# Kernel tuning notes

Measured on AMD Instinct MI355X. Metric: run time of the kernel, lower is better.

Reference implementation:

```python
import jax, jax.numpy as jnp
import numpy as np

B, S, H, A, E = 64, 1024, 1024, 512, 512


def setup_inputs() -> dict:
    key = jax.random.key(0)
    ks = jax.random.split(key, 13)
    sc = 0.02
    return {
        "inputs": jax.random.normal(ks[0], (B, E), jnp.float32),
        "states": jax.random.normal(ks[1], (B, H), jnp.float32),
        "encoded": jax.random.normal(ks[2], (B, S, H), jnp.float32),
        "W_enc": jax.random.normal(ks[3], (H, A), jnp.float32) * sc,
        "b_enc": jax.random.normal(ks[4], (A,), jnp.float32) * sc,
        "W_dec": jax.random.normal(ks[5], (H, A), jnp.float32) * sc,
        "b_dec": jax.random.normal(ks[6], (A,), jnp.float32) * sc,
        "w_out": jax.random.normal(ks[7], (A,), jnp.float32) * sc,
        "b_out": jax.random.normal(ks[8], (1,), jnp.float32) * sc,
        "W_ih": jax.random.normal(ks[9], (E + H, 3 * H), jnp.float32) * sc,
        "b_ih": jax.random.normal(ks[10], (3 * H,), jnp.float32) * sc,
        "W_hh": jax.random.normal(ks[11], (H, 3 * H), jnp.float32) * sc,
        "b_hh": jax.random.normal(ks[12], (3 * H,), jnp.float32) * sc,
    }


def reference(inputs, states, encoded, W_enc, b_enc, W_dec, b_dec, w_out, b_out,
              W_ih, b_ih, W_hh, b_hh):
    # setup_memory: project encoder states once  [B,S,H] @ [H,A] -> [B,S,A]
    enc_proj = jnp.einsum('bsh,ha->bsa', encoded, W_enc) + b_enc
    # Bahdanau additive attention
    dec_proj = states @ W_dec + b_dec                       # [B,A]
    scores = jnp.einsum('bsa,a->bs', jnp.tanh(enc_proj + dec_proj[:, None, :]), w_out) + b_out[0]
    weights = jax.nn.softmax(scores, axis=1)                # [B,S]
    attention = jnp.einsum('bs,bsh->bh', weights, encoded)  # [B,H]
    x = jnp.concatenate([inputs, attention], axis=-1)       # [B,E+H]
    # GRUCell (PyTorch gate order r, z, n)
    gi = x @ W_ih + b_ih                                    # [B,3H]
    gh = states @ W_hh + b_hh                               # [B,3H]
    i_r, i_z, i_n = jnp.split(gi, 3, axis=-1)
    h_r, h_z, h_n = jnp.split(gh, 3, axis=-1)
    r = jax.nn.sigmoid(i_r + h_r)
    z = jax.nn.sigmoid(i_z + h_z)
    n = jnp.tanh(i_n + r * h_n)
    h_new = (1.0 - z) * n + z * states
    return h_new
```

## Files before the change

kernel.cpp:

```cpp
#include <hip/hip_runtime.h>
#include <hip/hip_bf16.h>


typedef __attribute__((ext_vector_type(8))) __bf16 bf16x8;
typedef __attribute__((ext_vector_type(4))) __bf16 bf16x4;
typedef __attribute__((ext_vector_type(4))) float f32x4;

__device__ __forceinline__ float fast_tanh(float x) {
  float xa = fminf(fmaxf(x, -15.f), 15.f);
  float e = __expf(2.f * xa);
  return (e - 1.f) / (e + 1.f);
}

__global__ __launch_bounds__(256) void wenc_t_kernel(const float* __restrict__ W,
                                                     __bf16* __restrict__ Wt) {
  __shared__ float tile[32][33];
  int k0 = blockIdx.x * 32, a0 = blockIdx.y * 32;
  int tid = threadIdx.x;
  int r = tid >> 3, c4 = (tid & 7) * 4;
  f32x4 v = *(const f32x4*)(W + (long)(k0 + r) * 512 + a0 + c4);
  tile[r][c4 + 0] = v.x; tile[r][c4 + 1] = v.y;
  tile[r][c4 + 2] = v.z; tile[r][c4 + 3] = v.w;
  __syncthreads();
  int a = tid >> 3, k4 = (tid & 7) * 4;
  bf16x4 o = { (__bf16)tile[k4 + 0][a], (__bf16)tile[k4 + 1][a],
               (__bf16)tile[k4 + 2][a], (__bf16)tile[k4 + 3][a] };
  *(bf16x4*)(Wt + (long)(a0 + a) * 1024 + k0 + k4) = o;
}

__global__ __launch_bounds__(256) void dec_proj_kernel(
    const float* __restrict__ states, const float* __restrict__ W_dec,
    const float* __restrict__ b_enc, const float* __restrict__ b_dec,
    float* __restrict__ addv) {
  int b = blockIdx.x, tid = threadIdx.x;
  int a = blockIdx.y * 256 + tid;
  __shared__ float sl[1024];
  for (int i = tid; i < 1024; i += 256) sl[i] = states[b * 1024 + i];
  __syncthreads();
  float c0 = 0.f, c1 = 0.f, c2 = 0.f, c3 = 0.f;
#pragma unroll 4
  for (int i = 0; i < 256; ++i) {
    c0 += sl[i]         * W_dec[(i)        * 512 + a];
    c1 += sl[i + 256]   * W_dec[(i + 256)  * 512 + a];
    c2 += sl[i + 512]   * W_dec[(i + 512)  * 512 + a];
    c3 += sl[i + 768]   * W_dec[(i + 768)  * 512 + a];
  }
  addv[b * 512 + a] = c0 + c1 + c2 + c3 + b_enc[a] + b_dec[a];
}

struct Stage { f32x4 a[4]; bf16x8 b[2]; };

__global__ __launch_bounds__(512, 4) void enc_score_kernel(
    const float* __restrict__ encoded,
    const __bf16* __restrict__ Wt,
    const float* __restrict__ addv,
    const float* __restrict__ w_out,
    float* __restrict__ psc)
{
  __shared__ __attribute__((aligned(16))) char smem[65536];
  float* red = (float*)smem;

  const int d = blockIdx.x;
  const int xcd = d & 7;
  const int slot = d >> 3;
  const int bn = slot & 3;
  const int bm = ((slot >> 2) << 3) | xcd;

  const int tid = threadIdx.x;
  const int lane = tid & 63;
  const int wid = tid >> 6;
  const int wrow = wid >> 2;
  const int wcol = wid & 3;
  const int lr = lane & 15;
  const int lkb = lane >> 4;

  const long row0 = (long)bm * 128;
  const int col0 = bn * 128;

  const int arow = tid >> 2, akq = tid & 3;
  const int bcol = tid >> 2, bkq = tid & 3;
  const float* aBase = encoded + (row0 + arow) * 1024 + akq * 16;
  const __bf16* bBase = Wt + (long)(col0 + bcol) * 1024 + bkq * 16;
  const int asw = (arow & 7) << 4;
  const int aw0 = arow * 128 + ((akq * 32) ^ asw);
  const int aw1 = arow * 128 + ((akq * 32 + 16) ^ asw);
  const int bsw = (bcol & 7) << 4;
  const int bw0 = bcol * 128 + ((bkq * 32) ^ bsw);
  const int bw1 = bcol * 128 + ((bkq * 32 + 16) ^ bsw);

  const int rdSw = (lkb << 4) ^ ((lr & 7) << 4);
  const int aRow = (wrow * 64 + lr) * 128;
  const int bRow = (wcol * 32 + lr) * 128;

  f32x4 acc[4][2];
#pragma unroll
  for (int m = 0; m < 4; ++m)
#pragma unroll
    for (int n = 0; n < 2; ++n) acc[m][n] = (f32x4){0.f, 0.f, 0.f, 0.f};

  Stage X, Y;

#define ISSUE(S, KT) do { \
    _Pragma("unroll") for (int _j = 0; _j < 4; ++_j) \
      S.a[_j] = *(const f32x4*)(aBase + (KT) * 64 + _j * 4); \
    _Pragma("unroll") for (int _j = 0; _j < 2; ++_j) \
      S.b[_j] = *(const bf16x8*)(bBase + (KT) * 64 + _j * 8); \
    __builtin_amdgcn_sched_barrier(0); \
  } while (0)

#define STORE(S, ABUF) do { \
    bf16x8 _w0, _w1; \
    _Pragma("unroll") for (int _i = 0; _i < 4; ++_i) { \
      _w0[_i] = (__bf16)S.a[0][_i]; _w0[_i + 4] = (__bf16)S.a[1][_i]; \
      _w1[_i] = (__bf16)S.a[2][_i]; _w1[_i + 4] = (__bf16)S.a[3][_i]; } \
    *(bf16x8*)(smem + (ABUF) + aw0) = _w0; \
    *(bf16x8*)(smem + (ABUF) + aw1) = _w1; \
    *(bf16x8*)(smem + 32768 + (ABUF) + bw0) = S.b[0]; \
    *(bf16x8*)(smem + 32768 + (ABUF) + bw1) = S.b[1]; \
    __builtin_amdgcn_sched_barrier(0); \
  } while (0)

#define COMPUTE(ABUF) do { \
    _Pragma("unroll") for (int _ks = 0; _ks < 2; ++_ks) { \
      bf16x8 _af[4], _bf[2]; \
      _Pragma("unroll") for (int _m = 0; _m < 4; ++_m) \
        _af[_m] = *(const bf16x8*)(smem + (ABUF) + aRow + _m * 2048 + (rdSw ^ (_ks << 6))); \
      _Pragma("unroll") for (int _n = 0; _n < 2; ++_n) \
        _bf[_n] = *(const bf16x8*)(smem + 32768 + (ABUF) + bRow + _n * 2048 + (rdSw ^ (_ks << 6))); \
      asm volatile("s_waitcnt lgkmcnt(0)" ::: "memory"); \
      __builtin_amdgcn_sched_barrier(0); \
      __builtin_amdgcn_s_setprio(1); \
      _Pragma("unroll") for (int _m = 0; _m < 4; ++_m) \
        _Pragma("unroll") for (int _n = 0; _n < 2; ++_n) \
          acc[_m][_n] = __builtin_amdgcn_mfma_f32_16x16x32_bf16(_af[_m], _bf[_n], acc[_m][_n], 0, 0, 0); \
      __builtin_amdgcn_s_setprio(0); \
      __builtin_amdgcn_sched_barrier(0); \
    } \
  } while (0)

#define BAR() do { \
    asm volatile("s_waitcnt lgkmcnt(0)" ::: "memory"); \
    __builtin_amdgcn_sched_barrier(0); \
    __builtin_amdgcn_s_barrier(); \
    __builtin_amdgcn_sched_barrier(0); \
  } while (0)

  ISSUE(X, 0);
  ISSUE(Y, 1);
  STORE(X, 0);
  BAR();

  for (int t2 = 0; t2 < 7; ++t2) {
    ISSUE(X, 2 * t2 + 2);
    COMPUTE(0);
    STORE(Y, 16384);
    BAR();
    ISSUE(Y, 2 * t2 + 3);
    COMPUTE(16384);
    STORE(X, 0);
    BAR();
  }
  COMPUTE(0);
  STORE(Y, 16384);
  BAR();
  COMPUTE(16384);

#undef ISSUE
#undef STORE
#undef COMPUTE
#undef BAR

  const int b = bm >> 3;
  const float* addvb = addv + b * 512;
  float rowsum[4][4];
#pragma unroll
  for (int m = 0; m < 4; ++m)
#pragma unroll
    for (int reg = 0; reg < 4; ++reg) rowsum[m][reg] = 0.f;

#pragma unroll
  for (int m = 0; m < 4; ++m) {
#pragma unroll
    for (int n = 0; n < 2; ++n) {
      int col = col0 + wcol * 32 + n * 16 + lr;
      float av = addvb[col];
      float wo = w_out[col];
#pragma unroll
      for (int reg = 0; reg < 4; ++reg)
        rowsum[m][reg] += fast_tanh(acc[m][n][reg] + av) * wo;
    }
  }
#pragma unroll
  for (int m = 0; m < 4; ++m)
#pragma unroll
    for (int reg = 0; reg < 4; ++reg) {
      float v = rowsum[m][reg];
      v += __shfl_xor(v, 1, 64);
      v += __shfl_xor(v, 2, 64);
      v += __shfl_xor(v, 4, 64);
      v += __shfl_xor(v, 8, 64);
      rowsum[m][reg] = v;
    }
  if (lr == 0) {
#pragma unroll
    for (int m = 0; m < 4; ++m)
#pragma unroll
      for (int reg = 0; reg < 4; ++reg)
        red[(wrow * 64 + m * 16 + lkb * 4 + reg) * 4 + wcol] = rowsum[m][reg];
  }
  __syncthreads();
  if (tid < 128)
    psc[(long)bn * 65536 + row0 + tid] =
        red[tid * 4] + red[tid * 4 + 1] + red[tid * 4 + 2] + red[tid * 4 + 3];
}

__global__ __launch_bounds__(256) void softmax_kernel(const float* __restrict__ psc,
                                                      float* __restrict__ wts) {
  int b = blockIdx.x, tid = threadIdx.x;
  __shared__ float sred[8];
  float sc[4];
  float mx = -1e30f;
#pragma unroll
  for (int i = 0; i < 4; ++i) {
    long r = (long)b * 1024 + tid + i * 256;
    sc[i] = psc[r] + psc[65536 + r] + psc[2 * 65536 + r] + psc[3 * 65536 + r];
    mx = fmaxf(mx, sc[i]);
  }
  for (int off = 1; off < 64; off <<= 1) mx = fmaxf(mx, __shfl_xor(mx, off, 64));
  if ((tid & 63) == 0) sred[tid >> 6] = mx;
  __syncthreads();
  mx = fmaxf(fmaxf(sred[0], sred[1]), fmaxf(sred[2], sred[3]));
  float e[4], sum = 0.f;
#pragma unroll
  for (int i = 0; i < 4; ++i) {
    e[i] = __expf(sc[i] - mx);
    sum += e[i];
  }
  for (int off = 1; off < 64; off <<= 1) sum += __shfl_xor(sum, off, 64);
  if ((tid & 63) == 0) sred[4 + (tid >> 6)] = sum;
  __syncthreads();
  sum = sred[4] + sred[5] + sred[6] + sred[7];
  float inv = 1.f / sum;
#pragma unroll
  for (int i = 0; i < 4; ++i) wts[(long)b * 1024 + tid + i * 256] = e[i] * inv;
}

__global__ __launch_bounds__(256) void att_part_kernel(const float* __restrict__ encoded,
                                                       const float* __restrict__ wts,
                                                       float* __restrict__ attp) {
  int chunk = blockIdx.x;
  int b = blockIdx.y;
  int tid = threadIdx.x;
  f32x4 a0 = (f32x4){0.f, 0.f, 0.f, 0.f};
  f32x4 a1 = a0, a2 = a0, a3 = a0;
  const float* base = encoded + ((long)b * 1024 + chunk * 64) * 1024 + tid * 4;
  const float* w = wts + b * 1024 + chunk * 64;
#pragma unroll 4
  for (int s = 0; s < 64; s += 4) {
    f32x4 v0 = *(const f32x4*)(base + (long)(s + 0) * 1024);
    f32x4 v1 = *(const f32x4*)(base + (long)(s + 1) * 1024);
    f32x4 v2 = *(const f32x4*)(base + (long)(s + 2) * 1024);
    f32x4 v3 = *(const f32x4*)(base + (long)(s + 3) * 1024);
    a0 += v0 * w[s]; a1 += v1 * w[s + 1]; a2 += v2 * w[s + 2]; a3 += v3 * w[s + 3];
  }
  *(f32x4*)(attp + ((long)(b * 16 + chunk)) * 1024 + tid * 4) = (a0 + a1) + (a2 + a3);
}

__global__ __launch_bounds__(256) void xcat_kernel(const float* __restrict__ inputs,
                                                   const float* __restrict__ attp,
                                                   float* __restrict__ xcat) {
  int b = blockIdx.y;
  int k = blockIdx.x * 256 + threadIdx.x;
  float v;
  if (k < 512) {
    v = inputs[b * 512 + k];
  } else {
    int h = k - 512;
    v = 0.f;
#pragma unroll
    for (int c = 0; c < 16; ++c) v += attp[((long)(b * 16 + c)) * 1024 + h];
  }
  xcat[(long)b * 1536 + k] = v;
}

__global__ __launch_bounds__(512) void gru_gemv_kernel(
    const float* __restrict__ xcat, const float* __restrict__ states,
    const float* __restrict__ W_ih, const float* __restrict__ b_ih,
    const float* __restrict__ W_hh, const float* __restrict__ b_hh,
    float* __restrict__ gi, float* __restrict__ gh) {
  __shared__ float sx[12288];
  const int dd = blockIdx.x;
  const int xcd = dd & 7;
  const int n = dd >> 3;
  const int cgrp = xcd + 8 * (n >> 3);
  const int bg = n & 7;
  const int tid = threadIdx.x;
  const int lcol = tid & 255;
  const int bsel = (tid >> 8) * 4;

  if (cgrp < 12) {
    const int col = cgrp * 256 + lcol;
    const float* xb = xcat + (long)bg * 8 * 1536;
    for (int i = tid; i < 3072; i += 512) ((f32x4*)sx)[i] = ((const f32x4*)xb)[i];
    __syncthreads();
    float a0 = b_ih[col], a1 = a0, a2 = a0, a3 = a0;
    const float* x0 = sx + (bsel + 0) * 1536;
    const float* x1 = sx + (bsel + 1) * 1536;
    const float* x2 = sx + (bsel + 2) * 1536;
    const float* x3 = sx + (bsel + 3) * 1536;
    for (int k = 0; k < 1536; k += 4) {
      f32x4 v0 = *(const f32x4*)(x0 + k);
      f32x4 v1 = *(const f32x4*)(x1 + k);
      f32x4 v2 = *(const f32x4*)(x2 + k);
      f32x4 v3 = *(const f32x4*)(x3 + k);
#pragma unroll
      for (int j = 0; j < 4; ++j) {
        float w = W_ih[(long)(k + j) * 3072 + col];
        a0 += v0[j] * w; a1 += v1[j] * w; a2 += v2[j] * w; a3 += v3[j] * w;
      }
    }
    long o = (long)(bg * 8 + bsel) * 3072 + col;
    gi[o] = a0; gi[o + 3072] = a1; gi[o + 6144] = a2; gi[o + 9216] = a3;
  } else {
    const int col = (cgrp - 12) * 256 + lcol;
    const float* sb = states + (long)bg * 8 * 1024;
    for (int i = tid; i < 2048; i += 512) ((f32x4*)sx)[i] = ((const f32x4*)sb)[i];
    __syncthreads();
    float a0 = b_hh[col], a1 = a0, a2 = a0, a3 = a0;
    const float* x0 = sx + (bsel + 0) * 1024;
    const float* x1 = sx + (bsel + 1) * 1024;
    const float* x2 = sx + (bsel + 2) * 1024;
    const float* x3 = sx + (bsel + 3) * 1024;
    for (int k = 0; k < 1024; k += 4) {
      f32x4 v0 = *(const f32x4*)(x0 + k);
      f32x4 v1 = *(const f32x4*)(x1 + k);
      f32x4 v2 = *(const f32x4*)(x2 + k);
      f32x4 v3 = *(const f32x4*)(x3 + k);
#pragma unroll
      for (int j = 0; j < 4; ++j) {
        float w = W_hh[(long)(k + j) * 3072 + col];
        a0 += v0[j] * w; a1 += v1[j] * w; a2 += v2[j] * w; a3 += v3[j] * w;
      }
    }
    long o = (long)(bg * 8 + bsel) * 3072 + col;
    gh[o] = a0; gh[o + 3072] = a1; gh[o + 6144] = a2; gh[o + 9216] = a3;
  }
}

__global__ __launch_bounds__(256) void gate_kernel(const float* __restrict__ gi,
                                                   const float* __restrict__ gh,
                                                   const float* __restrict__ states,
                                                   float* __restrict__ out) {
  int b = blockIdx.y;
  int j = blockIdx.x * 256 + threadIdx.x;
  long o = (long)b * 3072;
  float ir = gi[o + j], hr = gh[o + j];
  float iz = gi[o + 1024 + j], hz = gh[o + 1024 + j];
  float in_ = gi[o + 2048 + j], hn = gh[o + 2048 + j];
  float r = 1.f / (1.f + __expf(-(ir + hr)));
  float z = 1.f / (1.f + __expf(-(iz + hz)));
  float n = fast_tanh(in_ + r * hn);
  out[(long)b * 1024 + j] = (1.f - z) * n + z * states[(long)b * 1024 + j];
}

extern "C" void kernel_launch(void* const* d_in, const int* in_sizes, int n_in,
                              void* d_out, int out_size, void* d_ws, size_t ws_size,
                              hipStream_t stream) {
  const float* inputs  = (const float*)d_in[0];
  const float* states  = (const float*)d_in[1];
  const float* encoded = (const float*)d_in[2];
  const float* W_enc   = (const float*)d_in[3];
  const float* b_enc   = (const float*)d_in[4];
  const float* W_dec   = (const float*)d_in[5];
  const float* b_dec   = (const float*)d_in[6];
  const float* w_out   = (const float*)d_in[7];
  const float* W_ih    = (const float*)d_in[9];
  const float* b_ih    = (const float*)d_in[10];
  const float* W_hh    = (const float*)d_in[11];
  const float* b_hh    = (const float*)d_in[12];
  float* out = (float*)d_out;
  float* ws = (float*)d_ws;

  float* addv = ws;
  float* psc  = ws + 32768;
  float* wts  = ws + 294912;
  float* attp = ws + 360448;
  float* xcat = ws + 1409024;
  float* gi   = ws + 1507328;
  float* gh   = ws + 1703936;
  __bf16* Wt  = (__bf16*)(ws + 1900544);

  wenc_t_kernel<<<dim3(32, 16), 256, 0, stream>>>(W_enc, Wt);

  dim3 gA(64, 2);
  dec_proj_kernel<<<gA, 256, 0, stream>>>(states, W_dec, b_enc, b_dec, addv);

  enc_score_kernel<<<2048, 512, 0, stream>>>(encoded, Wt, addv, w_out, psc);

  softmax_kernel<<<64, 256, 0, stream>>>(psc, wts);

  dim3 gD(16, 64);
  att_part_kernel<<<gD, 256, 0, stream>>>(encoded, wts, attp);

  dim3 gE(6, 64);
  xcat_kernel<<<gE, 256, 0, stream>>>(inputs, attp, xcat);

  gru_gemv_kernel<<<192, 512, 0, stream>>>(xcat, states, W_ih, b_ih, W_hh, b_hh, gi, gh);

  dim3 gG(4, 64);
  gate_kernel<<<gG, 256, 0, stream>>>(gi, gh, states, out);
}
```

Before: 327.2 us.

## Load encoder A-fragments directly from global into registers, stage only W_enc in LDS

The enc_score GEMM is restructured. Each wave now reads its encoder rows straight from global memory into MFMA A-fragments, converting fp32 to bf16 in registers. Only the W_enc^T tile (128 columns by 256 K per chunk) is staged in LDS with an XOR swizzle. Block tiles grow to 256 rows and the grid is halved, which removes the A-side LDS round trip and most barriers, at the cost of losing the explicit double-buffered prefetch and depending on uncoalesced-ish direct global loads for latency hiding.

```diff
diff --git a/kernel.cpp b/kernel.cpp
--- a/kernel.cpp
+++ b/kernel.cpp
@@ -48,8 +48,6 @@
   addv[b * 512 + a] = c0 + c1 + c2 + c3 + b_enc[a] + b_dec[a];
 }
 
-struct Stage { f32x4 a[4]; bf16x8 b[2]; };
-
 __global__ __launch_bounds__(512, 4) void enc_score_kernel(
     const float* __restrict__ encoded,
     const __bf16* __restrict__ Wt,
@@ -57,8 +55,8 @@
     const float* __restrict__ w_out,
     float* __restrict__ psc)
 {
-  __shared__ __attribute__((aligned(16))) char smem[65536];
-  float* red = (float*)smem;
+  __shared__ __attribute__((aligned(16))) char bsm[65536 + 1024];
+  float* red = (float*)(bsm + 65536);
 
   const int d = blockIdx.x;
   const int xcd = d & 7;
@@ -69,129 +67,87 @@
   const int tid = threadIdx.x;
   const int lane = tid & 63;
   const int wid = tid >> 6;
-  const int wrow = wid >> 2;
-  const int wcol = wid & 3;
   const int lr = lane & 15;
   const int lkb = lane >> 4;
 
-  const long row0 = (long)bm * 128;
+  const long row0 = (long)bm * 256;
   const int col0 = bn * 128;
 
-  const int arow = tid >> 2, akq = tid & 3;
-  const int bcol = tid >> 2, bkq = tid & 3;
-  const float* aBase = encoded + (row0 + arow) * 1024 + akq * 16;
-  const __bf16* bBase = Wt + (long)(col0 + bcol) * 1024 + bkq * 16;
-  const int asw = (arow & 7) << 4;
-  const int aw0 = arow * 128 + ((akq * 32) ^ asw);
-  const int aw1 = arow * 128 + ((akq * 32 + 16) ^ asw);
-  const int bsw = (bcol & 7) << 4;
-  const int bw0 = bcol * 128 + ((bkq * 32) ^ bsw);
-  const int bw1 = bcol * 128 + ((bkq * 32 + 16) ^ bsw);
-
-  const int rdSw = (lkb << 4) ^ ((lr & 7) << 4);
-  const int aRow = (wrow * 64 + lr) * 128;
-  const int bRow = (wcol * 32 + lr) * 128;
-
-  f32x4 acc[4][2];
-#pragma unroll
-  for (int m = 0; m < 4; ++m)
-#pragma unroll
-    for (int n = 0; n < 2; ++n) acc[m][n] = (f32x4){0.f, 0.f, 0.f, 0.f};
-
-  Stage X, Y;
-
-#define ISSUE(S, KT) do { \
-    _Pragma("unroll") for (int _j = 0; _j < 4; ++_j) \
-      S.a[_j] = *(const f32x4*)(aBase + (KT) * 64 + _j * 4); \
-    _Pragma("unroll") for (int _j = 0; _j < 2; ++_j) \
-      S.b[_j] = *(const bf16x8*)(bBase + (KT) * 64 + _j * 8); \
-    __builtin_amdgcn_sched_barrier(0); \
-  } while (0)
-
-#define STORE(S, ABUF) do { \
-    bf16x8 _w0, _w1; \
-    _Pragma("unroll") for (int _i = 0; _i < 4; ++_i) { \
-      _w0[_i] = (__bf16)S.a[0][_i]; _w0[_i + 4] = (__bf16)S.a[1][_i]; \
-      _w1[_i] = (__bf16)S.a[2][_i]; _w1[_i + 4] = (__bf16)S.a[3][_i]; } \
-    *(bf16x8*)(smem + (ABUF) + aw0) = _w0; \
-    *(bf16x8*)(smem + (ABUF) + aw1) = _w1; \
-    *(bf16x8*)(smem + 32768 + (ABUF) + bw0) = S.b[0]; \
-    *(bf16x8*)(smem + 32768 + (ABUF) + bw1) = S.b[1]; \
-    __builtin_amdgcn_sched_barrier(0); \
-  } while (0)
-
-#define COMPUTE(ABUF) do { \
-    _Pragma("unroll") for (int _ks = 0; _ks < 2; ++_ks) { \
-      bf16x8 _af[4], _bf[2]; \
-      _Pragma("unroll") for (int _m = 0; _m < 4; ++_m) \
-        _af[_m] = *(const bf16x8*)(smem + (ABUF) + aRow + _m * 2048 + (rdSw ^ (_ks << 6))); \
-      _Pragma("unroll") for (int _n = 0; _n < 2; ++_n) \
-        _bf[_n] = *(const bf16x8*)(smem + 32768 + (ABUF) + bRow + _n * 2048 + (rdSw ^ (_ks << 6))); \
-      asm volatile("s_waitcnt lgkmcnt(0)" ::: "memory"); \
-      __builtin_amdgcn_sched_barrier(0); \
-      __builtin_amdgcn_s_setprio(1); \
-      _Pragma("unroll") for (int _m = 0; _m < 4; ++_m) \
-        _Pragma("unroll") for (int _n = 0; _n < 2; ++_n) \
-          acc[_m][_n] = __builtin_amdgcn_mfma_f32_16x16x32_bf16(_af[_m], _bf[_n], acc[_m][_n], 0, 0, 0); \
-      __builtin_amdgcn_s_setprio(0); \
-      __builtin_amdgcn_sched_barrier(0); \
-    } \
-  } while (0)
-
-#define BAR() do { \
-    asm volatile("s_waitcnt lgkmcnt(0)" ::: "memory"); \
-    __builtin_amdgcn_sched_barrier(0); \
-    __builtin_amdgcn_s_barrier(); \
-    __builtin_amdgcn_sched_barrier(0); \
-  } while (0)
-
-  ISSUE(X, 0);
-  ISSUE(Y, 1);
-  STORE(X, 0);
-  BAR();
-
-  for (int t2 = 0; t2 < 7; ++t2) {
-    ISSUE(X, 2 * t2 + 2);
-    COMPUTE(0);
-    STORE(Y, 16384);
-    BAR();
-    ISSUE(Y, 2 * t2 + 3);
-    COMPUTE(16384);
-    STORE(X, 0);
-    BAR();
-  }
-  COMPUTE(0);
-  STORE(Y, 16384);
-  BAR();
-  COMPUTE(16384);
-
-#undef ISSUE
-#undef STORE
-#undef COMPUTE
-#undef BAR
-
-  const int b = bm >> 3;
+  const float* pa0 = encoded + (row0 + wid * 32 + lr) * 1024 + lkb * 8;
+  const float* pa1 = pa0 + 16 * 1024;
+
+  const int scol = tid >> 2;
+  const int skq = tid & 3;
+  const __bf16* wtb = Wt + (long)(col0 + scol) * 1024 + skq * 64;
+  const int ssw = (scol & 31) << 4;
+
+  const int rswE = lr << 4;
+  const int rswO = (lr << 4) | 256;
+  const int bB = lr * 512;
+
+  f32x4 acc[2][8];
+#pragma unroll
+  for (int m = 0; m < 2; ++m)
+#pragma unroll
+    for (int n = 0; n < 8; ++n) acc[m][n] = (f32x4){0.f, 0.f, 0.f, 0.f};
+
+  for (int ck = 0; ck < 4; ++ck) {
+    if (ck) __syncthreads();
+#pragma unroll
+    for (int j = 0; j < 8; ++j) {
+      bf16x8 v = *(const bf16x8*)(wtb + ck * 256 + j * 8);
+      *(bf16x8*)(bsm + scol * 512 + ((skq * 128 + j * 16) ^ ssw)) = v;
+    }
+    __syncthreads();
+
+#pragma unroll
+    for (int ktc = 0; ktc < 8; ++ktc) {
+      const int kt = ck * 8 + ktc;
+      f32x4 x0 = *(const f32x4*)(pa0 + kt * 32);
+      f32x4 x1 = *(const f32x4*)(pa0 + kt * 32 + 4);
+      f32x4 y0 = *(const f32x4*)(pa1 + kt * 32);
+      f32x4 y1 = *(const f32x4*)(pa1 + kt * 32 + 4);
+      bf16x8 a0, a1;
+#pragma unroll
+      for (int i = 0; i < 4; ++i) {
+        a0[i] = (__bf16)x0[i]; a0[4 + i] = (__bf16)x1[i];
+        a1[i] = (__bf16)y0[i]; a1[4 + i] = (__bf16)y1[i];
+      }
+      const int kbase = (ktc << 6) | (lkb << 4);
+      const int offE = kbase ^ rswE;
+      const int offO = kbase ^ rswO;
+      __builtin_amdgcn_s_setprio(1);
+#pragma unroll
+      for (int n = 0; n < 8; ++n) {
+        bf16x8 bf_ = *(const bf16x8*)(bsm + bB + n * 8192 + ((n & 1) ? offO : offE));
+        acc[0][n] = __builtin_amdgcn_mfma_f32_16x16x32_bf16(a0, bf_, acc[0][n], 0, 0, 0);
+        acc[1][n] = __builtin_amdgcn_mfma_f32_16x16x32_bf16(a1, bf_, acc[1][n], 0, 0, 0);
+      }
+      __builtin_amdgcn_s_setprio(0);
+    }
+  }
+
+  const int b = bm >> 2;
   const float* addvb = addv + b * 512;
-  float rowsum[4][4];
-#pragma unroll
-  for (int m = 0; m < 4; ++m)
+  float rowsum[2][4];
+#pragma unroll
+  for (int m = 0; m < 2; ++m)
 #pragma unroll
     for (int reg = 0; reg < 4; ++reg) rowsum[m][reg] = 0.f;
 
 #pragma unroll
-  for (int m = 0; m < 4; ++m) {
-#pragma unroll
-    for (int n = 0; n < 2; ++n) {
-      int col = col0 + wcol * 32 + n * 16 + lr;
-      float av = addvb[col];
-      float wo = w_out[col];
+  for (int n = 0; n < 8; ++n) {
+    int col = col0 + n * 16 + lr;
+    float av = addvb[col];
+    float wo = w_out[col];
+#pragma unroll
+    for (int m = 0; m < 2; ++m)
 #pragma unroll
       for (int reg = 0; reg < 4; ++reg)
         rowsum[m][reg] += fast_tanh(acc[m][n][reg] + av) * wo;
-    }
-  }
-#pragma unroll
-  for (int m = 0; m < 4; ++m)
+  }
+#pragma unroll
+  for (int m = 0; m < 2; ++m)
 #pragma unroll
     for (int reg = 0; reg < 4; ++reg) {
       float v = rowsum[m][reg];
@@ -201,17 +157,17 @@
       v += __shfl_xor(v, 8, 64);
       rowsum[m][reg] = v;
     }
+  __syncthreads();
   if (lr == 0) {
 #pragma unroll
-    for (int m = 0; m < 4; ++m)
+    for (int m = 0; m < 2; ++m)
 #pragma unroll
       for (int reg = 0; reg < 4; ++reg)
-        red[(wrow * 64 + m * 16 + lkb * 4 + reg) * 4 + wcol] = rowsum[m][reg];
-  }
-  __syncthreads();
-  if (tid < 128)
-    psc[(long)bn * 65536 + row0 + tid] =
-        red[tid * 4] + red[tid * 4 + 1] + red[tid * 4 + 2] + red[tid * 4 + 3];
+        red[wid * 32 + m * 16 + lkb * 4 + reg] = rowsum[m][reg];
+  }
+  __syncthreads();
+  if (tid < 256)
+    psc[(long)bn * 65536 + row0 + tid] = red[tid];
 }
 
 __global__ __launch_bounds__(256) void softmax_kernel(const float* __restrict__ psc,
@@ -395,7 +351,7 @@
   dim3 gA(64, 2);
   dec_proj_kernel<<<gA, 256, 0, stream>>>(states, W_dec, b_enc, b_dec, addv);
 
-  enc_score_kernel<<<2048, 512, 0, stream>>>(encoded, Wt, addv, w_out, psc);
+  enc_score_kernel<<<1024, 512, 0, stream>>>(encoded, Wt, addv, w_out, psc);
 
   softmax_kernel<<<64, 256, 0, stream>>>(psc, wts);
 
```

Result: slower. 396.4 us (+21.1%).
